# Kernel optimization log

Hardware: AMD Instinct MI355X
Metric: run time of the kernel (lower is better)

Reference implementation:

```python
import jax, jax.numpy as jnp
import numpy as np

B, IN, H, O, T = 4096, 128, 1024, 64, 25  # batch, static feat, hidden, outputs, steps


def setup_inputs() -> dict:
    key = jax.random.key(0)
    ks = jax.random.split(key, 11)
    s = 1.0 / np.sqrt(H)  # PyTorch LSTM/Linear uniform init scale
    u = lambda k, sh: jax.random.uniform(k, sh, jnp.float32, -s, s)
    return {
        "static_input": jax.random.normal(ks[0], (B, IN), jnp.float32),
        "W_ih0": u(ks[1], (4 * H, IN + O)),
        "W_hh0": u(ks[2], (4 * H, H)),
        "b_ih0": u(ks[3], (4 * H,)),
        "b_hh0": u(ks[4], (4 * H,)),
        "W_ih1": u(ks[5], (4 * H, H)),
        "W_hh1": u(ks[6], (4 * H, H)),
        "b_ih1": u(ks[7], (4 * H,)),
        "b_hh1": u(ks[8], (4 * H,)),
        "W_out": u(ks[9], (O, H)),
        "b_out": u(ks[10], (O,)),
        "num_steps": T,
    }


def _lstm_cell(x, h, c, W_ih, W_hh, b):
    # PyTorch gate order: input, forget, cell(g), output
    g = x @ W_ih.T + h @ W_hh.T + b
    i, f, gg, o = jnp.split(g, 4, axis=-1)
    c_new = jax.nn.sigmoid(f) * c + jax.nn.sigmoid(i) * jnp.tanh(gg)
    h_new = jax.nn.sigmoid(o) * jnp.tanh(c_new)
    return h_new, c_new


def reference(static_input, W_ih0, W_hh0, b_ih0, b_hh0,
              W_ih1, W_hh1, b_ih1, b_hh1, W_out, b_out, num_steps):
    b0 = b_ih0 + b_hh0
    b1 = b_ih1 + b_hh1
    batch = static_input.shape[0]
    hid = W_hh0.shape[1]
    out_dim = W_out.shape[0]
    z = jnp.zeros((batch, hid), jnp.float32)
    y0 = jnp.zeros((batch, out_dim), jnp.float32)  # output_seq[:, 0] is zeros at t=0

    def step(carry, _):
        h1, c1, h2, c2, y_prev = carry
        x = jnp.concatenate([static_input, y_prev], axis=-1)  # [B, IN+O]
        h1, c1 = _lstm_cell(x, h1, c1, W_ih0, W_hh0, b0)
        h2, c2 = _lstm_cell(h1, h2, c2, W_ih1, W_hh1, b1)
        y = h2 @ W_out.T + b_out  # [B, O]
        return (h1, c1, h2, c2, y), y

    _, ys = jax.lax.scan(step, (z, z, z, z, y0), None, length=num_steps)
    return jnp.transpose(ys, (1, 0, 2))  # [B, T, O]
```

## Files before the change

### kernel.cpp

```cpp
#include <hip/hip_runtime.h>

#define BATCH  4096
#define HID    1024
#define NOUT   64
#define TSTEPS 25
#define KA2    1280
#define KB     2048
#define LDY    1600

typedef __attribute__((ext_vector_type(8))) __bf16 bf16x8;
typedef __attribute__((ext_vector_type(4))) float  floatx4;

__device__ __forceinline__ unsigned short f2bf(float f) {
    union { float f; unsigned u; } v; v.f = f;
    unsigned r = v.u + 0x7fffu + ((v.u >> 16) & 1u);
    return (unsigned short)(r >> 16);
}
__device__ __forceinline__ float rcpf(float x) { return __builtin_amdgcn_rcpf(x); }
__device__ __forceinline__ float sigmf(float x) { return rcpf(1.0f + __expf(-x)); }
__device__ __forceinline__ float tanh_fast(float x) {
    float ax = fabsf(x);
    float e  = __expf(-2.0f * ax);
    float t  = (1.0f - e) * rcpf(1.0f + e);
    return copysignf(t, x);
}

#define GLDS16(gp, lp) __builtin_amdgcn_global_load_lds( \
    (const __attribute__((address_space(1))) void*)(gp), \
    (__attribute__((address_space(3))) void*)(lp), 16, 0, 0)

#define SB() __builtin_amdgcn_sched_barrier(0)

__global__ __launch_bounds__(512, 2) void lstm_gate_gemm(
    const unsigned short* __restrict__ X, int K,
    const unsigned short* __restrict__ W,
    const float* __restrict__ ginit,
    float* __restrict__ cell,
    unsigned short* __restrict__ d1, int ld1, int off1,
    unsigned short* __restrict__ d2, int ld2, int off2,
    float* __restrict__ dfp)
{
    __shared__ __align__(16) char smem[131072];

    const int tid  = threadIdx.x;
    const int lane = tid & 63;
    const int w    = tid >> 6;
    const int ql   = lane >> 4;
    const int lr   = lane & 15;
    const int wr   = w >> 2;
    const int wc   = w & 3;

    const int id  = blockIdx.y * 16 + blockIdx.x;
    const int xcd = id & 7;
    const int c   = id >> 3;
    const int bx  = (xcd & 3) * 4 + (c & 3);
    const int by  = (xcd >> 2) * 8 + (c >> 2);
    const int m0  = bx * 256;
    const int j0  = by * 64;

    const int s0  = w * 128 + lane;
    const int r0  = s0 >> 3;
    const int kc0 = (s0 & 7) ^ (r0 & 7);
    const unsigned sOff = (unsigned)s0 * 16;
    const unsigned short* sA[2];
    const unsigned short* sB[2];
    sA[0] = X + (size_t)(m0 + r0) * K + kc0 * 8;
    sA[1] = X + (size_t)(m0 + 128 + r0) * K + kc0 * 8;
    {
        const int nb0 = r0, nb1 = 128 + r0;
        sB[0] = W + (size_t)((nb0 & 3) * HID + j0 + (nb0 >> 2)) * K + kc0 * 8;
        sB[1] = W + (size_t)((nb1 & 3) * HID + j0 + (nb1 >> 2)) * K + kc0 * 8;
    }

#define STAGE_A(h, tt, p) do { \
    const unsigned short* _s = sA[h] + (size_t)(tt) * 64; \
    char* _d = smem + (p) + (h) * 16384 + sOff; \
    GLDS16(_s, _d); \
    GLDS16(_s + 8 * (size_t)K, _d + 1024); \
} while (0)

#define STAGE_B(h, tt, p) do { \
    const unsigned short* _s = sB[h] + (size_t)(tt) * 64; \
    char* _d = smem + (p) + 32768 + (h) * 16384 + sOff; \
    GLDS16(_s, _d); \
    GLDS16(_s + 2 * (size_t)K, _d + 1024); \
} while (0)

    unsigned offA[4], offB[2];
#pragma unroll
    for (int fi = 0; fi < 4; ++fi) {
        int r = wr * 64 + fi * 16 + lr;
        offA[fi] = (unsigned)((r * 8 + (ql ^ (r & 7))) * 16);
    }
#pragma unroll
    for (int fj = 0; fj < 2; ++fj) {
        int r = wc * 32 + fj * 16 + lr;
        offB[fj] = (unsigned)(32768 + (r * 8 + (ql ^ (r & 7))) * 16);
    }

#define LOAD_A(AV, BASE) do { \
    const char* _ab = smem + (BASE); \
    _Pragma("unroll") \
    for (int fi = 0; fi < 4; ++fi) { \
        AV[fi][0] = *(const bf16x8*)(_ab + offA[fi]); \
        AV[fi][1] = *(const bf16x8*)(_ab + (offA[fi] ^ 64u)); \
    } \
} while (0)

#define LOAD_B(BV, BASE) do { \
    const char* _bb = smem + (BASE); \
    _Pragma("unroll") \
    for (int fj = 0; fj < 2; ++fj) { \
        BV[fj][0] = *(const bf16x8*)(_bb + offB[fj]); \
        BV[fj][1] = *(const bf16x8*)(_bb + (offB[fj] ^ 64u)); \
    } \
} while (0)

#define MFMA_PART(Q, AV, BV, F0, F1) do { \
    __builtin_amdgcn_s_setprio(1); \
    _Pragma("unroll") \
    for (int kk = 0; kk < 2; ++kk) \
    _Pragma("unroll") \
    for (int fi = (F0); fi < (F1); ++fi) \
    _Pragma("unroll") \
    for (int fj = 0; fj < 2; ++fj) \
        acc[Q][fi][fj] = __builtin_amdgcn_mfma_f32_16x16x32_bf16( \
            AV[fi][kk], BV[fj][kk], acc[Q][fi][fj], 0, 0, 0); \
    __builtin_amdgcn_s_setprio(0); \
} while (0)

    floatx4 acc[4][4][2];
#pragma unroll
    for (int q = 0; q < 4; ++q)
#pragma unroll
        for (int i = 0; i < 4; ++i)
#pragma unroll
            for (int j = 0; j < 2; ++j)
                acc[q][i][j] = floatx4{0.f, 0.f, 0.f, 0.f};

    const int NT = K >> 6;

    bf16x8 av0[4][2], av1[4][2], bv0[2][2], bv1[2][2];

    STAGE_B(1, 0, 0); STAGE_A(1, 0, 0); STAGE_A(0, 0, 0); STAGE_B(0, 0, 0);
    STAGE_B(1, 1, 65536); STAGE_A(1, 1, 65536); STAGE_A(0, 1, 65536); STAGE_B(0, 1, 65536);
    asm volatile("s_waitcnt vmcnt(8)");
    __builtin_amdgcn_s_barrier();
    SB();
    LOAD_A(av0, 0);
    LOAD_B(bv0, 0);
    LOAD_B(bv1, 16384);
    SB();

    int par = 0;
    for (int t = 0; t < NT; ++t) {
        const int cur = par << 16;
        const int np  = cur ^ 65536;
        const int t2  = (t + 2 < NT) ? t + 2 : NT - 1;
        __builtin_amdgcn_s_barrier();
        SB();
        MFMA_PART(0, av0, bv0, 0, 1);
        SB();
        LOAD_A(av1, cur + 16384);
        STAGE_B(1, t2, cur);
        SB();
        MFMA_PART(0, av0, bv0, 1, 4);
        SB();
        __builtin_amdgcn_s_barrier();
        SB();
        MFMA_PART(1, av0, bv1, 0, 1);
        SB();
        STAGE_A(1, t2, cur);
        SB();
        MFMA_PART(1, av0, bv1, 1, 4);
        SB();
        asm volatile("s_waitcnt vmcnt(6)");
        __builtin_amdgcn_s_barrier();
        SB();
        MFMA_PART(2, av1, bv1, 0, 1);
        SB();
        LOAD_A(av0, np);
        STAGE_A(0, t2, cur);
        SB();
        MFMA_PART(2, av1, bv1, 1, 4);
        SB();
        asm volatile("s_waitcnt vmcnt(6)");
        __builtin_amdgcn_s_barrier();
        SB();
        MFMA_PART(3, av1, bv0, 0, 1);
        SB();
        LOAD_B(bv1, np + 16384);
        STAGE_B(0, t2, cur);
        SB();
        MFMA_PART(3, av1, bv0, 1, 4);
        SB();
        LOAD_B(bv0, np);
        par ^= 1;
    }

    asm volatile("s_waitcnt vmcnt(0)");
    __builtin_amdgcn_s_barrier();

    float* scratch = (float*)(void*)smem + w * 640;
    const int jj   = lane & 7;
    const int rsel = lane >> 3;

    float  cpre[4][4][2];
    float4 gi4[4];
#pragma unroll
    for (int qd = 0; qd < 4; ++qd) {
        const int qa = (qd >= 2) ? 1 : 0;
        const int qb = (qd == 1 || qd == 2) ? 1 : 0;
        const int rowbase = m0 + qa * 128 + wr * 64;
        const int jg = j0 + qb * 32 + wc * 8 + jj;
        gi4[qd] = *(const float4*)(ginit + (size_t)jg * 4);
#pragma unroll
        for (int fi = 0; fi < 4; ++fi)
#pragma unroll
            for (int p = 0; p < 2; ++p)
                cpre[qd][fi][p] = cell[(size_t)(rowbase + fi * 16 + rsel + p * 8) * HID + jg];
    }

#pragma unroll
    for (int qd = 0; qd < 4; ++qd) {
        const int qa = (qd >= 2) ? 1 : 0;
        const int qb = (qd == 1 || qd == 2) ? 1 : 0;
        const int rowbase = m0 + qa * 128 + wr * 64;
        const int jg = j0 + qb * 32 + wc * 8 + jj;
        const float4 gi = gi4[qd];
#pragma unroll
        for (int fi = 0; fi < 4; ++fi) {
#pragma unroll
            for (int fj = 0; fj < 2; ++fj)
#pragma unroll
                for (int r = 0; r < 4; ++r)
                    scratch[(ql * 4 + r) * 36 + fj * 16 + lr] = acc[qd][fi][fj][r];
            asm volatile("" ::: "memory");
#pragma unroll
            for (int p = 0; p < 2; ++p) {
                const int row = rsel + p * 8;
                const float4 g = *(const float4*)(scratch + row * 36 + jj * 4);
                const int b = rowbase + fi * 16 + row;
                float iv = sigmf(g.x + gi.x);
                float fv = sigmf(g.y + gi.y);
                float gv = tanh_fast(g.z + gi.z);
                float ov = sigmf(g.w + gi.w);
                size_t ci = (size_t)b * HID + jg;
                float cn = fv * cpre[qd][fi][p] + iv * gv;
                cell[ci] = cn;
                float hv = ov * tanh_fast(cn);
                unsigned short hb = f2bf(hv);
                d1[(size_t)b * ld1 + off1 + jg] = hb;
                if (d2)  d2[(size_t)b * ld2 + off2 + jg] = hb;
                if (dfp) dfp[(size_t)b * HID + jg] = hv;
            }
            asm volatile("" ::: "memory");
        }
    }
#undef MFMA_PART
#undef LOAD_A
#undef LOAD_B
#undef STAGE_A
#undef STAGE_B
}

__global__ __launch_bounds__(256) void out_gemm(
    const float* __restrict__ h2, const float* __restrict__ wt,
    const float* __restrict__ bout, float* __restrict__ y,
    unsigned short* __restrict__ xn)
{
    __shared__ float hl[16 * 1024];
    const int tid = threadIdx.x;
    const int b0 = blockIdx.x * 16;
#pragma unroll
    for (int r = 0; r < 16; ++r) {
        int f4 = r * 256 + tid;
        *(float4*)(hl + f4 * 4) = *(const float4*)(h2 + (size_t)b0 * 1024 + f4 * 4);
    }
    __syncthreads();
    const int o  = tid & 63;
    const int wv = tid >> 6;
    float a0 = 0.f, a1 = 0.f, a2 = 0.f, a3 = 0.f;
#pragma unroll 8
    for (int k = 0; k < 1024; ++k) {
        float wvv = wt[k * 64 + o];
        const float* hr = hl + (wv * 4) * 1024 + k;
        a0 += hr[0]    * wvv;
        a1 += hr[1024] * wvv;
        a2 += hr[2048] * wvv;
        a3 += hr[3072] * wvv;
    }
    float bo = bout[o];
    int b = b0 + wv * 4;
    float yv[4] = {a0 + bo, a1 + bo, a2 + bo, a3 + bo};
#pragma unroll
    for (int r = 0; r < 4; ++r) {
        y[(size_t)(b + r) * LDY + o] = yv[r];
        xn[(size_t)(b + r) * KA2 + o] = f2bf(yv[r]);
    }
}

__global__ void build_woutT(const float* __restrict__ wout, float* __restrict__ wt)
{
    int idx = blockIdx.x * 256 + threadIdx.x;
    int o = idx & 63, k = idx >> 6;
    wt[idx] = wout[(size_t)o * 1024 + k];
}

__global__ void build_bias(const float* __restrict__ a, const float* __restrict__ b,
                           float* __restrict__ o)
{
    int idx = blockIdx.x * 256 + threadIdx.x;
    int gate = idx & 3, j = idx >> 2;
    int n = gate * 1024 + j;
    o[idx] = a[n] + b[n];
}

__global__ __launch_bounds__(256) void build_w0(
    const float* __restrict__ wih, const float* __restrict__ whh,
    unsigned short* __restrict__ w0)
{
    int idx = blockIdx.x * 256 + threadIdx.x;
    int n = idx / 320;
    int c = (idx - n * 320) * 4;
    float4 v = {0.f, 0.f, 0.f, 0.f};
    if (c < 64)        v = *(const float4*)(wih + (size_t)n * 192 + 128 + c);
    else if (c < 192)  v = *(const float4*)(wih + (size_t)n * 192 + (c - 64));
    else if (c < 1216) v = *(const float4*)(whh + (size_t)n * 1024 + (c - 192));
    ushort4 o;
    o.x = f2bf(v.x); o.y = f2bf(v.y); o.z = f2bf(v.z); o.w = f2bf(v.w);
    *(ushort4*)(w0 + (size_t)n * KA2 + c) = o;
}

__global__ __launch_bounds__(256) void build_w1(
    const float* __restrict__ wih, const float* __restrict__ whh,
    unsigned short* __restrict__ w1)
{
    int idx = blockIdx.x * 256 + threadIdx.x;
    int n = idx >> 9;
    int c = (idx & 511) * 4;
    float4 v;
    if (c < 1024) v = *(const float4*)(wih + (size_t)n * 1024 + c);
    else          v = *(const float4*)(whh + (size_t)n * 1024 + (c - 1024));
    ushort4 o;
    o.x = f2bf(v.x); o.y = f2bf(v.y); o.z = f2bf(v.z); o.w = f2bf(v.w);
    *(ushort4*)(w1 + (size_t)n * KB + c) = o;
}

__global__ __launch_bounds__(256) void build_x0static(
    const float* __restrict__ stat, unsigned short* __restrict__ xa,
    unsigned short* __restrict__ xb)
{
    int idx = blockIdx.x * 256 + threadIdx.x;
    int b = idx >> 5;
    int c = (idx & 31) * 4;
    float4 v = *(const float4*)(stat + (size_t)b * 128 + c);
    ushort4 o;
    o.x = f2bf(v.x); o.y = f2bf(v.y); o.z = f2bf(v.z); o.w = f2bf(v.w);
    *(ushort4*)(xa + (size_t)b * KA2 + 64 + c) = o;
    *(ushort4*)(xb + (size_t)b * KA2 + 64 + c) = o;
}

extern "C" void kernel_launch(void* const* d_in, const int* in_sizes, int n_in,
                              void* d_out, int out_size, void* d_ws, size_t ws_size,
                              hipStream_t stream)
{
    (void)in_sizes; (void)n_in; (void)out_size; (void)ws_size;
    const float* static_in = (const float*)d_in[0];
    const float* Wih0 = (const float*)d_in[1];
    const float* Whh0 = (const float*)d_in[2];
    const float* bih0 = (const float*)d_in[3];
    const float* bhh0 = (const float*)d_in[4];
    const float* Wih1 = (const float*)d_in[5];
    const float* Whh1 = (const float*)d_in[6];
    const float* bih1 = (const float*)d_in[7];
    const float* bhh1 = (const float*)d_in[8];
    const float* Wout = (const float*)d_in[9];
    const float* bout = (const float*)d_in[10];
    float* out = (float*)d_out;

    char* p = (char*)d_ws;
    size_t off = 0;
    auto take = [&](size_t n) { char* r = p + off; off += (n + 255) & ~(size_t)255; return r; };

    unsigned short* W0   = (unsigned short*)take((size_t)4096 * KA2 * 2);
    unsigned short* W1   = (unsigned short*)take((size_t)4096 * KB * 2);
    float*          B1b  = (float*)take(4096 * 4);
    float*          B0b  = (float*)take(4096 * 4);
    float*          WoT  = (float*)take((size_t)1024 * 64 * 4);
    float*          H2f  = (float*)take((size_t)BATCH * HID * 4);
    float*          C1   = (float*)take((size_t)BATCH * HID * 4);
    float*          C2   = (float*)take((size_t)BATCH * HID * 4);
    unsigned short* X0a  = (unsigned short*)take((size_t)BATCH * KA2 * 2);
    unsigned short* X0b  = (unsigned short*)take((size_t)BATCH * KA2 * 2);
    unsigned short* X1a  = (unsigned short*)take((size_t)BATCH * KB * 2);
    unsigned short* X1b  = (unsigned short*)take((size_t)BATCH * KB * 2);

    hipMemsetAsync(C1, 0, (size_t)BATCH * HID * 4, stream);
    hipMemsetAsync(C2, 0, (size_t)BATCH * HID * 4, stream);
    hipMemsetAsync(X0a, 0, (size_t)BATCH * KA2 * 2, stream);
    hipMemsetAsync(X0b, 0, (size_t)BATCH * KA2 * 2, stream);
    hipMemsetAsync(X1a, 0, (size_t)BATCH * KB * 2, stream);

    build_w0<<<5120, 256, 0, stream>>>(Wih0, Whh0, W0);
    build_w1<<<8192, 256, 0, stream>>>(Wih1, Whh1, W1);
    build_woutT<<<256, 256, 0, stream>>>(Wout, WoT);
    build_bias<<<16, 256, 0, stream>>>(bih0, bhh0, B0b);
    build_bias<<<16, 256, 0, stream>>>(bih1, bhh1, B1b);
    build_x0static<<<512, 256, 0, stream>>>(static_in, X0a, X0b);

    dim3 grid(16, 16);
    for (int t = 0; t < TSTEPS; ++t) {
        unsigned short* X0c = (t & 1) ? X0b : X0a;
        unsigned short* X0n = (t & 1) ? X0a : X0b;
        unsigned short* X1c = (t & 1) ? X1b : X1a;
        unsigned short* X1n = (t & 1) ? X1a : X1b;
        lstm_gate_gemm<<<grid, 512, 0, stream>>>(X0c, KA2, W0, B0b, C1,
                                                 X1c, KB, 0, X0n, KA2, 192, nullptr);
        lstm_gate_gemm<<<grid, 512, 0, stream>>>(X1c, KB, W1, B1b, C2,
                                                 X1n, KB, 1024, nullptr, 0, 0, H2f);
        out_gemm<<<256, 256, 0, stream>>>(H2f, WoT, bout, out + t * NOUT, X0n);
    }
}
```

Baseline: 3.668 ms.

## Fuse output projection into layer-1 gate kernel and trim padded K

Removes the separate out_gemm launch each step. The layer-1 LSTM gate kernel now waits on a per-row-block atomic counter until all 16 column blocks have written h2, then computes the 64-wide output projection and writes y and the bf16 feedback. The layer-0 input layout is reordered (static, h1, y) so the GEMM can loop over only 1216 of the 1280 padded K columns. The MFMA loop nest order is also changed. The spin-wait depends on all blocks in a row group being resident at the same time and adds global atomics.

```diff
diff --git a/kernel.cpp b/kernel.cpp
--- a/kernel.cpp
+++ b/kernel.cpp
@@ -5,6 +5,7 @@
 #define NOUT   64
 #define TSTEPS 25
 #define KA2    1280
+#define KT0    1216
 #define KB     2048
 #define LDY    1600
 
@@ -32,13 +33,16 @@
 #define SB() __builtin_amdgcn_sched_barrier(0)
 
 __global__ __launch_bounds__(512, 2) void lstm_gate_gemm(
-    const unsigned short* __restrict__ X, int K,
+    const unsigned short* __restrict__ X, int K, int Kt,
     const unsigned short* __restrict__ W,
     const float* __restrict__ ginit,
     float* __restrict__ cell,
     unsigned short* __restrict__ d1, int ld1, int off1,
     unsigned short* __restrict__ d2, int ld2, int off2,
-    float* __restrict__ dfp)
+    float* __restrict__ dfp,
+    const float* __restrict__ wt, const float* __restrict__ bo,
+    float* __restrict__ yout, unsigned short* __restrict__ xnY,
+    unsigned* cnt)
 {
     __shared__ __align__(16) char smem[131072];
 
@@ -119,11 +123,11 @@
 #define MFMA_PART(Q, AV, BV, F0, F1) do { \
     __builtin_amdgcn_s_setprio(1); \
     _Pragma("unroll") \
-    for (int kk = 0; kk < 2; ++kk) \
-    _Pragma("unroll") \
     for (int fi = (F0); fi < (F1); ++fi) \
     _Pragma("unroll") \
     for (int fj = 0; fj < 2; ++fj) \
+    _Pragma("unroll") \
+    for (int kk = 0; kk < 2; ++kk) \
         acc[Q][fi][fj] = __builtin_amdgcn_mfma_f32_16x16x32_bf16( \
             AV[fi][kk], BV[fj][kk], acc[Q][fi][fj], 0, 0, 0); \
     __builtin_amdgcn_s_setprio(0); \
@@ -138,7 +142,7 @@
             for (int j = 0; j < 2; ++j)
                 acc[q][i][j] = floatx4{0.f, 0.f, 0.f, 0.f};
 
-    const int NT = K >> 6;
+    const int NT = Kt >> 6;
 
     bf16x8 av0[4][2], av1[4][2], bv0[2][2], bv1[2][2];
 
@@ -257,6 +261,42 @@
             asm volatile("" ::: "memory");
         }
     }
+
+    if (wt) {
+        __syncthreads();
+        if (tid == 0) {
+            __hip_atomic_fetch_add(&cnt[bx], 1u, __ATOMIC_RELEASE, __HIP_MEMORY_SCOPE_AGENT);
+            while (__hip_atomic_load(&cnt[bx], __ATOMIC_RELAXED, __HIP_MEMORY_SCOPE_AGENT) < 16u)
+                __builtin_amdgcn_s_sleep(2);
+        }
+        __syncthreads();
+
+        float* hl = (float*)(void*)smem;
+        const int rb = m0 + by * 16;
+#pragma unroll
+        for (int r = 0; r < 8; ++r) {
+            int f4 = r * 512 + tid;
+            *(float4*)(hl + f4 * 4) = *(const float4*)(dfp + (size_t)rb * 1024 + f4 * 4);
+        }
+        __syncthreads();
+        const int o  = tid & 63;
+        const int wv = tid >> 6;
+        float a0 = 0.f, a1 = 0.f;
+#pragma unroll 8
+        for (int k = 0; k < 1024; ++k) {
+            float wvv = wt[k * 64 + o];
+            const float* hr = hl + (wv * 2) * 1024 + k;
+            a0 += hr[0]    * wvv;
+            a1 += hr[1024] * wvv;
+        }
+        float bb = bo[o];
+        int b = rb + wv * 2;
+        float y0 = a0 + bb, y1 = a1 + bb;
+        yout[(size_t)b * LDY + o] = y0;
+        yout[(size_t)(b + 1) * LDY + o] = y1;
+        xnY[(size_t)b * KA2 + 1152 + o] = f2bf(y0);
+        xnY[(size_t)(b + 1) * KA2 + 1152 + o] = f2bf(y1);
+    }
 #undef MFMA_PART
 #undef LOAD_A
 #undef LOAD_B
@@ -264,42 +304,6 @@
 #undef STAGE_B
 }
 
-__global__ __launch_bounds__(256) void out_gemm(
-    const float* __restrict__ h2, const float* __restrict__ wt,
-    const float* __restrict__ bout, float* __restrict__ y,
-    unsigned short* __restrict__ xn)
-{
-    __shared__ float hl[16 * 1024];
-    const int tid = threadIdx.x;
-    const int b0 = blockIdx.x * 16;
-#pragma unroll
-    for (int r = 0; r < 16; ++r) {
-        int f4 = r * 256 + tid;
-        *(float4*)(hl + f4 * 4) = *(const float4*)(h2 + (size_t)b0 * 1024 + f4 * 4);
-    }
-    __syncthreads();
-    const int o  = tid & 63;
-    const int wv = tid >> 6;
-    float a0 = 0.f, a1 = 0.f, a2 = 0.f, a3 = 0.f;
-#pragma unroll 8
-    for (int k = 0; k < 1024; ++k) {
-        float wvv = wt[k * 64 + o];
-        const float* hr = hl + (wv * 4) * 1024 + k;
-        a0 += hr[0]    * wvv;
-        a1 += hr[1024] * wvv;
-        a2 += hr[2048] * wvv;
-        a3 += hr[3072] * wvv;
-    }
-    float bo = bout[o];
-    int b = b0 + wv * 4;
-    float yv[4] = {a0 + bo, a1 + bo, a2 + bo, a3 + bo};
-#pragma unroll
-    for (int r = 0; r < 4; ++r) {
-        y[(size_t)(b + r) * LDY + o] = yv[r];
-        xn[(size_t)(b + r) * KA2 + o] = f2bf(yv[r]);
-    }
-}
-
 __global__ void build_woutT(const float* __restrict__ wout, float* __restrict__ wt)
 {
     int idx = blockIdx.x * 256 + threadIdx.x;
@@ -324,9 +328,9 @@
     int n = idx / 320;
     int c = (idx - n * 320) * 4;
     float4 v = {0.f, 0.f, 0.f, 0.f};
-    if (c < 64)        v = *(const float4*)(wih + (size_t)n * 192 + 128 + c);
-    else if (c < 192)  v = *(const float4*)(wih + (size_t)n * 192 + (c - 64));
-    else if (c < 1216) v = *(const float4*)(whh + (size_t)n * 1024 + (c - 192));
+    if (c < 128)       v = *(const float4*)(wih + (size_t)n * 192 + c);
+    else if (c < 1152) v = *(const float4*)(whh + (size_t)n * 1024 + (c - 128));
+    else if (c < 1216) v = *(const float4*)(wih + (size_t)n * 192 + 128 + (c - 1152));
     ushort4 o;
     o.x = f2bf(v.x); o.y = f2bf(v.y); o.z = f2bf(v.z); o.w = f2bf(v.w);
     *(ushort4*)(w0 + (size_t)n * KA2 + c) = o;
@@ -357,8 +361,8 @@
     float4 v = *(const float4*)(stat + (size_t)b * 128 + c);
     ushort4 o;
     o.x = f2bf(v.x); o.y = f2bf(v.y); o.z = f2bf(v.z); o.w = f2bf(v.w);
-    *(ushort4*)(xa + (size_t)b * KA2 + 64 + c) = o;
-    *(ushort4*)(xb + (size_t)b * KA2 + 64 + c) = o;
+    *(ushort4*)(xa + (size_t)b * KA2 + c) = o;
+    *(ushort4*)(xb + (size_t)b * KA2 + c) = o;
 }
 
 extern "C" void kernel_launch(void* const* d_in, const int* in_sizes, int n_in,
@@ -395,12 +399,14 @@
     unsigned short* X0b  = (unsigned short*)take((size_t)BATCH * KA2 * 2);
     unsigned short* X1a  = (unsigned short*)take((size_t)BATCH * KB * 2);
     unsigned short* X1b  = (unsigned short*)take((size_t)BATCH * KB * 2);
+    unsigned*       cnt  = (unsigned*)take(TSTEPS * 16 * 4);
 
     hipMemsetAsync(C1, 0, (size_t)BATCH * HID * 4, stream);
     hipMemsetAsync(C2, 0, (size_t)BATCH * HID * 4, stream);
     hipMemsetAsync(X0a, 0, (size_t)BATCH * KA2 * 2, stream);
     hipMemsetAsync(X0b, 0, (size_t)BATCH * KA2 * 2, stream);
     hipMemsetAsync(X1a, 0, (size_t)BATCH * KB * 2, stream);
+    hipMemsetAsync(cnt, 0, TSTEPS * 16 * 4, stream);
 
     build_w0<<<5120, 256, 0, stream>>>(Wih0, Whh0, W0);
     build_w1<<<8192, 256, 0, stream>>>(Wih1, Whh1, W1);
@@ -415,10 +421,12 @@
         unsigned short* X0n = (t & 1) ? X0a : X0b;
         unsigned short* X1c = (t & 1) ? X1b : X1a;
         unsigned short* X1n = (t & 1) ? X1a : X1b;
-        lstm_gate_gemm<<<grid, 512, 0, stream>>>(X0c, KA2, W0, B0b, C1,
-                                                 X1c, KB, 0, X0n, KA2, 192, nullptr);
-        lstm_gate_gemm<<<grid, 512, 0, stream>>>(X1c, KB, W1, B1b, C2,
-                                                 X1n, KB, 1024, nullptr, 0, 0, H2f);
-        out_gemm<<<256, 256, 0, stream>>>(H2f, WoT, bout, out + t * NOUT, X0n);
-    }
-}
+        lstm_gate_gemm<<<grid, 512, 0, stream>>>(X0c, KA2, KT0, W0, B0b, C1,
+                                                 X1c, KB, 0, X0n, KA2, 128, nullptr,
+                                                 nullptr, nullptr, nullptr, nullptr, nullptr);
+        lstm_gate_gemm<<<grid, 512, 0, stream>>>(X1c, KB, KB, W1, B1b, C2,
+                                                 X1n, KB, 1024, nullptr, 0, 0, H2f,
+                                                 WoT, bout, out + t * NOUT, X0n,
+                                                 cnt + t * 16);
+    }
+}
```

After: 4.097 ms. 1.12x slower.
